# Kernel optimization log

Measured on AMD Instinct MI355X. Metric: run time of the kernel, lower is better.

The kernel has to match this reference:

```python
import jax, jax.numpy as jnp
import numpy as np

S = 4096      # total packed tokens
B = 8         # number of variable-length segments
E = 1152      # embed_dim (SigLIP2 so400m)
H = 16        # num_heads
D = E // H    # head_dim = 72


def setup_inputs() -> dict:
    key = jax.random.key(0)
    ks = jax.random.split(key, 8)
    w_std = 0.02
    theta = jax.random.uniform(ks[1], (S, D), jnp.float32, 0.0, 2.0 * np.pi)
    return {
        "hidden_states": jax.random.normal(ks[0], (S, E), jnp.float32),
        "cu_seqlens": jnp.arange(B + 1, dtype=jnp.int32) * (S // B),
        "cos": jnp.cos(theta),
        "sin": jnp.sin(theta),
        "Wq": jax.random.normal(ks[2], (E, E), jnp.float32) * w_std,
        "bq": jnp.zeros((E,), jnp.float32),
        "Wk": jax.random.normal(ks[3], (E, E), jnp.float32) * w_std,
        "bk": jnp.zeros((E,), jnp.float32),
        "Wv": jax.random.normal(ks[4], (E, E), jnp.float32) * w_std,
        "bv": jnp.zeros((E,), jnp.float32),
        "Wo": jax.random.normal(ks[5], (E, E), jnp.float32) * w_std,
        "bo": jnp.zeros((E,), jnp.float32),
    }


def _rotate_half(x):
    x1, x2 = jnp.split(x, 2, axis=-1)
    return jnp.concatenate((-x2, x1), axis=-1)


def reference(hidden_states, cu_seqlens, cos, sin, Wq, bq, Wk, bk, Wv, bv, Wo, bo):
    seq_len = hidden_states.shape[0]
    scale = np.float32(D) ** -0.5
    # projections -> [S, H, D]
    q = (hidden_states @ Wq.T + bq).reshape(seq_len, H, D)
    k = (hidden_states @ Wk.T + bk).reshape(seq_len, H, D)
    v = (hidden_states @ Wv.T + bv).reshape(seq_len, H, D)
    # inline RoPE (apply_rotary_pos_emb_vision): cos/sin broadcast over heads
    c = cos[:, None, :]
    s = sin[:, None, :]
    q = q * c + _rotate_half(q) * s
    k = k * c + _rotate_half(k) * s
    # segment id per token from cu_seqlens; block-diagonal attention mask
    seg = jnp.searchsorted(cu_seqlens[1:], jnp.arange(seq_len, dtype=cu_seqlens.dtype), side="right")
    mask = seg[:, None] == seg[None, :]                     # [S, S]
    scores = jnp.einsum("shd,thd->hst", q, k) * scale       # [H, S, S]
    neg = jnp.finfo(scores.dtype).min
    scores = jnp.where(mask[None, :, :], scores, neg)
    probs = jax.nn.softmax(scores, axis=-1)
    attn = jnp.einsum("hst,thd->shd", probs, v).reshape(seq_len, E)
    return attn @ Wo.T + bo
```

## Files before the change

### kernel.cpp

```cpp
#include <hip/hip_runtime.h>
#include <float.h>

#define S_LEN 4096
#define E_DIM 1152
#define NH    16
#define HD    72
#define HD2   36
#define NQKV  3456

typedef __attribute__((ext_vector_type(4))) float f32x4;
typedef __attribute__((ext_vector_type(8))) _Float16 f16x8;

__device__ __forceinline__ unsigned short f2h(float f) {
    union { _Float16 h; unsigned short u; } c;
    c.h = (_Float16)f;
    return c.u;
}

__device__ __forceinline__ void gload_lds16(const unsigned short* g, unsigned short* l) {
    __builtin_amdgcn_global_load_lds(
        (const __attribute__((address_space(1))) unsigned int*)g,
        (__attribute__((address_space(3))) unsigned int*)l, 16, 0, 0);
}

__global__ __launch_bounds__(256)
void pack_f16(const float* __restrict__ hs, const float* __restrict__ wq,
              const float* __restrict__ wk, const float* __restrict__ wv,
              const float* __restrict__ wo,
              unsigned short* __restrict__ hs_h, unsigned short* __restrict__ wqkv_h,
              unsigned short* __restrict__ wo_h)
{
    const float* src; unsigned short* dst; int n4;
    const int WSZ = E_DIM * E_DIM;
    switch (blockIdx.z) {
        case 0: src = hs; dst = hs_h;             n4 = S_LEN * E_DIM / 4; break;
        case 1: src = wq; dst = wqkv_h;           n4 = WSZ / 4; break;
        case 2: src = wk; dst = wqkv_h + WSZ;     n4 = WSZ / 4; break;
        case 3: src = wv; dst = wqkv_h + 2 * WSZ; n4 = WSZ / 4; break;
        default: src = wo; dst = wo_h;            n4 = WSZ / 4; break;
    }
    for (int i = blockIdx.x * 256 + threadIdx.x; i < n4; i += gridDim.x * 256) {
        f32x4 x = ((const f32x4*)src)[i];
        ushort4 hv;
        hv.x = f2h(x[0]); hv.y = f2h(x[1]); hv.z = f2h(x[2]); hv.w = f2h(x[3]);
        ((ushort4*)dst)[i] = hv;
    }
}

__global__ __launch_bounds__(256, 4)
void gemm_qkv_f16(const unsigned short* __restrict__ Ah, const unsigned short* __restrict__ Wh,
                  const float* __restrict__ bq, const float* __restrict__ bk,
                  const float* __restrict__ bv,
                  float* __restrict__ oq, float* __restrict__ ok, float* __restrict__ ov)
{
    __shared__ unsigned short sA[128 * 64];
    __shared__ unsigned short sB[128 * 64];
    const int tid  = threadIdx.x;
    const int w    = tid >> 6, lane = tid & 63;
    const int quad = lane >> 4, m = lane & 15;
    const int wr   = w & 1,  wc = w >> 1;

    const int bid = blockIdx.x;
    const int lin = (bid & 7) * 108 + (bid >> 3);
    const int n_t = lin >> 5;
    const int m_t = lin & 31;
    const int m0  = m_t * 128;
    const int n0  = n_t * 128;

    const int srow = lane >> 3;
    const int skc  = (lane & 7) ^ srow;

    f32x4 acc[4][4];
    #pragma unroll
    for (int i = 0; i < 4; ++i)
        #pragma unroll
        for (int j = 0; j < 4; ++j) acc[i][j] = (f32x4){0.f, 0.f, 0.f, 0.f};

    const int rm7 = m & 7;

    for (int k0 = 0; k0 < E_DIM; k0 += 64) {
        #pragma unroll
        for (int c = 0; c < 4; ++c) {
            int r = 32 * w + 8 * c + srow;
            gload_lds16(Ah + (size_t)(m0 + r) * E_DIM + k0 + skc * 8, &sA[(32 * w + 8 * c) * 64]);
            gload_lds16(Wh + (size_t)(n0 + r) * E_DIM + k0 + skc * 8, &sB[(32 * w + 8 * c) * 64]);
        }
        __syncthreads();

        #pragma unroll
        for (int k3 = 0; k3 < 2; ++k3) {
            f16x8 ah[4], bh[4];
            #pragma unroll
            for (int t = 0; t < 4; ++t) {
                int pc = ((k3 << 2) + quad) ^ rm7;
                ah[t] = *(const f16x8*)&sA[(64 * wr + 16 * t + m) * 64 + pc * 8];
                bh[t] = *(const f16x8*)&sB[(64 * wc + 16 * t + m) * 64 + pc * 8];
            }
            #pragma unroll
            for (int rt = 0; rt < 4; ++rt)
                #pragma unroll
                for (int ct = 0; ct < 4; ++ct)
                    acc[rt][ct] = __builtin_amdgcn_mfma_f32_16x16x32_f16(ah[rt], bh[ct], acc[rt][ct], 0, 0, 0);
        }
        __syncthreads();
    }

    const int which = n0 / E_DIM;
    const int n0l = n0 - which * E_DIM;
    const float* bp = (which == 0) ? bq : (which == 1) ? bk : bv;
    float* Cp       = (which == 0) ? oq : (which == 1) ? ok : ov;
    #pragma unroll
    for (int ct = 0; ct < 4; ++ct) {
        int col = n0l + 64 * wc + 16 * ct + m;
        float bias = bp[col];
        #pragma unroll
        for (int rt = 0; rt < 4; ++rt)
            #pragma unroll
            for (int reg = 0; reg < 4; ++reg) {
                int row = m0 + 64 * wr + 16 * rt + 4 * quad + reg;
                Cp[(size_t)row * E_DIM + col] = acc[rt][ct][reg] + bias;
            }
    }
}

__global__ __launch_bounds__(256, 4)
void gemm_out_f16(const unsigned short* __restrict__ Ah, const unsigned short* __restrict__ Wh,
                  const float* __restrict__ bo, float* __restrict__ Cp)
{
    __shared__ unsigned short sA[64 * 64];
    __shared__ unsigned short sB[128 * 64];
    const int tid  = threadIdx.x;
    const int w    = tid >> 6, lane = tid & 63;
    const int quad = lane >> 4, m = lane & 15;
    const int m0   = blockIdx.y * 64;
    const int n0   = blockIdx.x * 128;

    const int srow = lane >> 3;
    const int skc  = (lane & 7) ^ srow;

    f32x4 acc[4][2];
    #pragma unroll
    for (int i = 0; i < 4; ++i)
        #pragma unroll
        for (int j = 0; j < 2; ++j) acc[i][j] = (f32x4){0.f, 0.f, 0.f, 0.f};

    const int rm7 = m & 7;

    for (int k0 = 0; k0 < E_DIM; k0 += 64) {
        #pragma unroll
        for (int c = 0; c < 2; ++c) {
            int r = 16 * w + 8 * c + srow;
            gload_lds16(Ah + (size_t)(m0 + r) * E_DIM + k0 + skc * 8, &sA[(16 * w + 8 * c) * 64]);
        }
        #pragma unroll
        for (int c = 0; c < 4; ++c) {
            int r = 32 * w + 8 * c + srow;
            gload_lds16(Wh + (size_t)(n0 + r) * E_DIM + k0 + skc * 8, &sB[(32 * w + 8 * c) * 64]);
        }
        __syncthreads();
        #pragma unroll
        for (int k3 = 0; k3 < 2; ++k3) {
            f16x8 ah[4], bh[2];
            int pc = ((k3 << 2) + quad) ^ rm7;
            #pragma unroll
            for (int t = 0; t < 4; ++t)
                ah[t] = *(const f16x8*)&sA[(16 * t + m) * 64 + pc * 8];
            #pragma unroll
            for (int ct = 0; ct < 2; ++ct)
                bh[ct] = *(const f16x8*)&sB[(32 * w + 16 * ct + m) * 64 + pc * 8];
            #pragma unroll
            for (int rt = 0; rt < 4; ++rt)
                #pragma unroll
                for (int ct = 0; ct < 2; ++ct)
                    acc[rt][ct] = __builtin_amdgcn_mfma_f32_16x16x32_f16(ah[rt], bh[ct], acc[rt][ct], 0, 0, 0);
        }
        __syncthreads();
    }

    #pragma unroll
    for (int ct = 0; ct < 2; ++ct) {
        int col = n0 + 32 * w + 16 * ct + m;
        float bias = bo[col];
        #pragma unroll
        for (int rt = 0; rt < 4; ++rt)
            #pragma unroll
            for (int reg = 0; reg < 4; ++reg) {
                int row = m0 + 16 * rt + 4 * quad + reg;
                Cp[(size_t)row * E_DIM + col] = acc[rt][ct][reg] + bias;
            }
    }
}

__global__ __launch_bounds__(256)
void prep_kv(const float* __restrict__ kf, const float* __restrict__ vf,
             const float* __restrict__ cosb, const float* __restrict__ sinb,
             unsigned short* __restrict__ kh, unsigned short* __restrict__ vt)
{
    __shared__ unsigned short tile[HD][72];
    const int h  = blockIdx.y;
    const int s0 = blockIdx.x * 64;

    if (blockIdx.z == 0) {
        for (int task = threadIdx.x; task < 64 * 9; task += 256) {
            int row = task / 9, d0 = (task % 9) << 2;
            int s = s0 + row;
            const float* xr = kf + (size_t)s * E_DIM + h * HD;
            f32x4 a  = *(const f32x4*)(xr + d0);
            f32x4 b  = *(const f32x4*)(xr + d0 + HD2);
            f32x4 c1 = *(const f32x4*)(cosb + (size_t)s * HD + d0);
            f32x4 s1 = *(const f32x4*)(sinb + (size_t)s * HD + d0);
            f32x4 c2 = *(const f32x4*)(cosb + (size_t)s * HD + d0 + HD2);
            f32x4 s2 = *(const f32x4*)(sinb + (size_t)s * HD + d0 + HD2);
            f32x4 r1 = a * c1 - b * s1;
            f32x4 r2 = b * c2 + a * s2;
            uint2 u1, u2;
            u1.x = (unsigned)f2h(r1[0]) | ((unsigned)f2h(r1[1]) << 16);
            u1.y = (unsigned)f2h(r1[2]) | ((unsigned)f2h(r1[3]) << 16);
            u2.x = (unsigned)f2h(r2[0]) | ((unsigned)f2h(r2[1]) << 16);
            u2.y = (unsigned)f2h(r2[2]) | ((unsigned)f2h(r2[3]) << 16);
            unsigned short* orow = kh + ((size_t)h * S_LEN + s) * HD;
            *(uint2*)&orow[d0]       = u1;
            *(uint2*)&orow[d0 + HD2] = u2;
        }
    } else {
        for (int task = threadIdx.x; task < 64 * 18; task += 256) {
            int r = task / 18, c = task % 18;
            f32x4 x = *(const f32x4*)(vf + (size_t)(s0 + r) * E_DIM + h * HD + (c << 2));
            tile[(c << 2) + 0][r] = f2h(x[0]);
            tile[(c << 2) + 1][r] = f2h(x[1]);
            tile[(c << 2) + 2][r] = f2h(x[2]);
            tile[(c << 2) + 3][r] = f2h(x[3]);
        }
        __syncthreads();
        for (int task = threadIdx.x; task < HD * 8; task += 256) {
            int d = task / 8, cc = task % 8;
            uint4 val = *(const uint4*)&tile[d][cc << 3];
            *(uint4*)(vt + ((size_t)h * HD + d) * S_LEN + s0 + (cc << 3)) = val;
        }
    }
}

__global__ __launch_bounds__(256, 4)
void attn_f16(const float* __restrict__ qf, const float* __restrict__ cosb,
              const float* __restrict__ sinb, const unsigned short* __restrict__ kh,
              const unsigned short* __restrict__ vt, const int* __restrict__ cu,
              int nseg, unsigned short* __restrict__ out)
{
    __shared__ unsigned short ks_s[64][72];
    __shared__ unsigned short vs_s[80][72];
    __shared__ unsigned short ss_s[64][72];

    const int tid  = threadIdx.x;
    const int w    = tid >> 6;
    const int lane = tid & 63;
    const int quad = lane >> 4;
    const int m    = lane & 15;
    const int h    = blockIdx.y;
    const int qb0  = blockIdx.x * 64;
    const float cexp = 0.17002324f;

    {
        uint4 zz = make_uint4(0u, 0u, 0u, 0u);
        if (tid < 72) {
            int r = 72 + tid / 9, c = tid % 9;
            *(uint4*)&vs_s[r][c << 3] = zz;
        }
    }

    int rs_r[4], re_r[4];
    #pragma unroll
    for (int reg = 0; reg < 4; ++reg) {
        int row = qb0 + 16 * w + 4 * quad + reg;
        int st = 0;
        for (int i = 1; i < nseg; ++i) if (cu[i] <= row) st = i;
        rs_r[reg] = cu[st];
        re_r[reg] = cu[st + 1];
    }
    int st0 = 0, st1 = 0;
    for (int i = 1; i < nseg; ++i) {
        if (cu[i] <= qb0) st0 = i;
        if (cu[i] <= qb0 + 63) st1 = i;
    }
    const int kstart = cu[st0];
    const int kend   = cu[st1 + 1];
    const bool aligned = (st0 == st1);

    const unsigned short* ktbase = kh + (size_t)h * S_LEN * HD;
    const unsigned short* vtbase = vt + (size_t)h * HD * S_LEN;
    unsigned short* ksf = &ks_s[0][0];

    const int sl0 = tid, sl1 = tid + 256;
    const int sl2 = (tid < 64) ? tid + 512 : tid + 256;
    const int vd0 = sl0 >> 3, vc0 = (sl0 & 7) << 3;
    const int vd1 = sl1 >> 3, vc1 = (sl1 & 7) << 3;
    const int vd2 = sl2 >> 3, vc2 = (sl2 & 7) << 3;

    uint4 kp0, kp1, kp2, vp0, vp1, vp2;
    {
        const unsigned short* kt = ktbase + (size_t)kstart * HD;
        kp0 = *(const uint4*)(kt + sl0 * 8);
        kp1 = *(const uint4*)(kt + sl1 * 8);
        kp2 = *(const uint4*)(kt + sl2 * 8);
        vp0 = *(const uint4*)(vtbase + (size_t)vd0 * S_LEN + kstart + vc0);
        vp1 = *(const uint4*)(vtbase + (size_t)vd1 * S_LEN + kstart + vc1);
        vp2 = *(const uint4*)(vtbase + (size_t)vd2 * S_LEN + kstart + vc2);
    }

    for (int task = tid; task < 64 * 9; task += 256) {
        int row = task / 9, d0 = (task % 9) << 2;
        int s = qb0 + row;
        const float* xr = qf + (size_t)s * E_DIM + h * HD;
        f32x4 a  = *(const f32x4*)(xr + d0);
        f32x4 b  = *(const f32x4*)(xr + d0 + HD2);
        f32x4 c1 = *(const f32x4*)(cosb + (size_t)s * HD + d0);
        f32x4 s1 = *(const f32x4*)(sinb + (size_t)s * HD + d0);
        f32x4 c2 = *(const f32x4*)(cosb + (size_t)s * HD + d0 + HD2);
        f32x4 s2 = *(const f32x4*)(sinb + (size_t)s * HD + d0 + HD2);
        f32x4 r1 = a * c1 - b * s1;
        f32x4 r2 = b * c2 + a * s2;
        uint2 u1, u2;
        u1.x = (unsigned)f2h(r1[0]) | ((unsigned)f2h(r1[1]) << 16);
        u1.y = (unsigned)f2h(r1[2]) | ((unsigned)f2h(r1[3]) << 16);
        u2.x = (unsigned)f2h(r2[0]) | ((unsigned)f2h(r2[1]) << 16);
        u2.y = (unsigned)f2h(r2[2]) | ((unsigned)f2h(r2[3]) << 16);
        *(uint2*)&ks_s[row][d0]       = u1;
        *(uint2*)&ks_s[row][d0 + HD2] = u2;
    }
    __syncthreads();

    f16x8 qfr[3];
    {
        const unsigned short* qrow = &ks_s[16 * w + m][0];
        #pragma unroll
        for (int k3 = 0; k3 < 3; ++k3) {
            bool pad = (k3 == 2) && (quad != 0);
            int off = pad ? 0 : (k3 * 32 + quad * 8);
            f16x8 val = *(const f16x8*)(qrow + off);
            f16x8 z = {0, 0, 0, 0, 0, 0, 0, 0};
            qfr[k3] = pad ? z : val;
        }
    }

    f32x4 acc_o[5];
    #pragma unroll
    for (int i = 0; i < 5; ++i) acc_o[i] = (f32x4){0.f, 0.f, 0.f, 0.f};
    float l_r[4] = {0.f, 0.f, 0.f, 0.f};

    for (int kb = kstart; kb < kend; kb += 64) {
        __syncthreads();
        *(uint4*)(ksf + sl0 * 8) = kp0;
        *(uint4*)(ksf + sl1 * 8) = kp1;
        if (tid < 64) *(uint4*)(ksf + sl2 * 8) = kp2;
        *(uint4*)&vs_s[vd0][vc0] = vp0;
        *(uint4*)&vs_s[vd1][vc1] = vp1;
        if (tid < 64) *(uint4*)&vs_s[vd2][vc2] = vp2;
        __syncthreads();

        int kn = kb + 64;
        if (kn < kend) {
            const unsigned short* kt = ktbase + (size_t)kn * HD;
            kp0 = *(const uint4*)(kt + sl0 * 8);
            kp1 = *(const uint4*)(kt + sl1 * 8);
            kp2 = *(const uint4*)(kt + sl2 * 8);
            vp0 = *(const uint4*)(vtbase + (size_t)vd0 * S_LEN + kn + vc0);
            vp1 = *(const uint4*)(vtbase + (size_t)vd1 * S_LEN + kn + vc1);
            vp2 = *(const uint4*)(vtbase + (size_t)vd2 * S_LEN + kn + vc2);
        }

        f32x4 sacc[4];
        #pragma unroll
        for (int ct = 0; ct < 4; ++ct) sacc[ct] = (f32x4){0.f, 0.f, 0.f, 0.f};
        #pragma unroll
        for (int ct = 0; ct < 4; ++ct) {
            const unsigned short* krow = &ks_s[16 * ct + m][0];
            #pragma unroll
            for (int k3 = 0; k3 < 3; ++k3) {
                bool pad = (k3 == 2) && (quad != 0);
                int off = pad ? 0 : (k3 * 32 + quad * 8);
                f16x8 bfr = *(const f16x8*)(krow + off);
                f16x8 z = {0, 0, 0, 0, 0, 0, 0, 0};
                bfr = pad ? z : bfr;
                sacc[ct] = __builtin_amdgcn_mfma_f32_16x16x32_f16(qfr[k3], bfr, sacc[ct], 0, 0, 0);
            }
        }

        if (aligned) {
            #pragma unroll
            for (int ct = 0; ct < 4; ++ct)
                #pragma unroll
                for (int reg = 0; reg < 4; ++reg) {
                    float p = __builtin_amdgcn_exp2f(sacc[ct][reg] * cexp);
                    l_r[reg] += p;
                    ss_s[16 * w + 4 * quad + reg][16 * ct + m] = f2h(p);
                }
        } else {
            #pragma unroll
            for (int ct = 0; ct < 4; ++ct) {
                int key = kb + 16 * ct + m;
                #pragma unroll
                for (int reg = 0; reg < 4; ++reg) {
                    bool valid = (key >= rs_r[reg]) && (key < re_r[reg]);
                    float p = valid ? __builtin_amdgcn_exp2f(sacc[ct][reg] * cexp) : 0.f;
                    l_r[reg] += p;
                    ss_s[16 * w + 4 * quad + reg][16 * ct + m] = f2h(p);
                }
            }
        }

        {
            const unsigned short* prow = &ss_s[16 * w + m][0];
            f16x8 pf0 = *(const f16x8*)(prow + quad * 8);
            f16x8 pf1 = *(const f16x8*)(prow + 32 + quad * 8);
            #pragma unroll
            for (int ct2 = 0; ct2 < 5; ++ct2) {
                const unsigned short* vrow = &vs_s[16 * ct2 + m][0];
                f16x8 vf0 = *(const f16x8*)(vrow + quad * 8);
                f16x8 vf1 = *(const f16x8*)(vrow + 32 + quad * 8);
                acc_o[ct2] = __builtin_amdgcn_mfma_f32_16x16x32_f16(pf0, vf0, acc_o[ct2], 0, 0, 0);
                acc_o[ct2] = __builtin_amdgcn_mfma_f32_16x16x32_f16(pf1, vf1, acc_o[ct2], 0, 0, 0);
            }
        }
    }

    #pragma unroll
    for (int reg = 0; reg < 4; ++reg) {
        float l = l_r[reg];
        l += __shfl_xor(l, 1);
        l += __shfl_xor(l, 2);
        l += __shfl_xor(l, 4);
        l += __shfl_xor(l, 8);
        l_r[reg] = l;
    }

    #pragma unroll
    for (int reg = 0; reg < 4; ++reg) {
        float linv = (l_r[reg] > 0.f) ? 1.f / l_r[reg] : 0.f;
        int row = qb0 + 16 * w + 4 * quad + reg;
        unsigned short* orow = out + (size_t)row * E_DIM + h * HD;
        #pragma unroll
        for (int ct2 = 0; ct2 < 5; ++ct2) {
            int col = 16 * ct2 + m;
            if (col < HD) orow[col] = f2h(acc_o[ct2][reg] * linv);
        }
    }
}

extern "C" void kernel_launch(void* const* d_in, const int* in_sizes, int n_in,
                              void* d_out, int out_size, void* d_ws, size_t ws_size,
                              hipStream_t stream)
{
    const float* hs   = (const float*)d_in[0];
    const int*   cu   = (const int*)d_in[1];
    const float* cosb = (const float*)d_in[2];
    const float* sinb = (const float*)d_in[3];
    const float* Wq   = (const float*)d_in[4];
    const float* bq   = (const float*)d_in[5];
    const float* Wk   = (const float*)d_in[6];
    const float* bk   = (const float*)d_in[7];
    const float* Wv   = (const float*)d_in[8];
    const float* bv   = (const float*)d_in[9];
    const float* Wo   = (const float*)d_in[10];
    const float* bo   = (const float*)d_in[11];
    float* outp = (float*)d_out;

    const size_t mat = (size_t)S_LEN * E_DIM;
    float* qf = (float*)d_ws;
    float* kf = qf + mat;
    float* vf = kf + mat;
    unsigned short* hs_h   = (unsigned short*)(vf + mat);
    unsigned short* wqkv_h = hs_h + mat;
    unsigned short* wo_h   = wqkv_h + (size_t)NQKV * E_DIM;
    unsigned short* vtb    = wo_h + (size_t)E_DIM * E_DIM;
    unsigned short* kh     = hs_h;
    unsigned short* attn_h = (unsigned short*)vf;

    const int nseg = in_sizes[1] - 1;

    dim3 gpack(512, 1, 5);
    pack_f16<<<gpack, 256, 0, stream>>>(hs, Wq, Wk, Wv, Wo, hs_h, wqkv_h, wo_h);

    gemm_qkv_f16<<<dim3(864), 256, 0, stream>>>(hs_h, wqkv_h, bq, bk, bv, qf, kf, vf);

    dim3 gprep(S_LEN / 64, NH, 2);
    prep_kv<<<gprep, 256, 0, stream>>>(kf, vf, cosb, sinb, kh, vtb);

    dim3 gattn(S_LEN / 64, NH, 1);
    attn_f16<<<gattn, 256, 0, stream>>>(qf, cosb, sinb, kh, vtb, cu, nseg, attn_h);

    dim3 gout(E_DIM / 128, S_LEN / 64, 1);
    gemm_out_f16<<<gout, 256, 0, stream>>>(attn_h, wo_h, bo, outp);
}
```

Measured before the change: 208.7 us.

## Rewrite QKV GEMM with 256x256 double-buffered tiles and a fused QKV output layout

The QKV projection GEMM now uses 512-thread blocks computing 256x256 tiles, with double-buffered LDS so the next K-slice's global-to-LDS loads overlap the current MFMA work. It uses explicit vmcnt waits, barriers and s_setprio around the MFMA bursts. Q, K and V are written into a single interleaved [S, 3456] fp32 buffer. The attention output is placed in the already-consumed V columns with a matching stride, and downstream kernels are re-indexed accordingly. The larger LDS footprint (about 128KB) limits each CU to one block, and the last N tile is partly wasted on padding rows.

```diff
diff --git a/kernel.cpp b/kernel.cpp
--- a/kernel.cpp
+++ b/kernel.cpp
@@ -7,6 +7,8 @@
 #define HD    72
 #define HD2   36
 #define NQKV  3456
+#define QKVP  3456
+#define AH_STRIDE 6912
 
 typedef __attribute__((ext_vector_type(4))) float f32x4;
 typedef __attribute__((ext_vector_type(8))) _Float16 f16x8;
@@ -47,79 +49,107 @@
     }
 }
 
-__global__ __launch_bounds__(256, 4)
-void gemm_qkv_f16(const unsigned short* __restrict__ Ah, const unsigned short* __restrict__ Wh,
+__global__ __launch_bounds__(512, 2)
+void gemm_qkv_8ph(const unsigned short* __restrict__ Ah, const unsigned short* __restrict__ Wh,
                   const float* __restrict__ bq, const float* __restrict__ bk,
-                  const float* __restrict__ bv,
-                  float* __restrict__ oq, float* __restrict__ ok, float* __restrict__ ov)
+                  const float* __restrict__ bv, float* __restrict__ C)
 {
-    __shared__ unsigned short sA[128 * 64];
-    __shared__ unsigned short sB[128 * 64];
+    __shared__ unsigned short sA[2][256 * 64];
+    __shared__ unsigned short sB[2][256 * 64];
+
     const int tid  = threadIdx.x;
     const int w    = tid >> 6, lane = tid & 63;
     const int quad = lane >> 4, m = lane & 15;
-    const int wr   = w & 1,  wc = w >> 1;
+    const int wm   = w >> 2,  wn = w & 3;
 
     const int bid = blockIdx.x;
-    const int lin = (bid & 7) * 108 + (bid >> 3);
-    const int n_t = lin >> 5;
-    const int m_t = lin & 31;
-    const int m0  = m_t * 128;
-    const int n0  = n_t * 128;
+    const int lin = (bid & 7) * 28 + (bid >> 3);
+    const int n_t = lin >> 4;
+    const int m_t = lin & 15;
+    const int m0  = m_t * 256;
+    const int n0  = n_t * 256;
 
     const int srow = lane >> 3;
     const int skc  = (lane & 7) ^ srow;
-
-    f32x4 acc[4][4];
-    #pragma unroll
-    for (int i = 0; i < 4; ++i)
+    const int rm7  = m & 7;
+
+    f32x4 acc[8][4];
+    #pragma unroll
+    for (int i = 0; i < 8; ++i)
         #pragma unroll
         for (int j = 0; j < 4; ++j) acc[i][j] = (f32x4){0.f, 0.f, 0.f, 0.f};
 
-    const int rm7 = m & 7;
-
-    for (int k0 = 0; k0 < E_DIM; k0 += 64) {
-        #pragma unroll
-        for (int c = 0; c < 4; ++c) {
-            int r = 32 * w + 8 * c + srow;
-            gload_lds16(Ah + (size_t)(m0 + r) * E_DIM + k0 + skc * 8, &sA[(32 * w + 8 * c) * 64]);
-            gload_lds16(Wh + (size_t)(n0 + r) * E_DIM + k0 + skc * 8, &sB[(32 * w + 8 * c) * 64]);
-        }
-        __syncthreads();
-
-        #pragma unroll
-        for (int k3 = 0; k3 < 2; ++k3) {
-            f16x8 ah[4], bh[4];
-            #pragma unroll
-            for (int t = 0; t < 4; ++t) {
-                int pc = ((k3 << 2) + quad) ^ rm7;
-                ah[t] = *(const f16x8*)&sA[(64 * wr + 16 * t + m) * 64 + pc * 8];
-                bh[t] = *(const f16x8*)&sB[(64 * wc + 16 * t + m) * 64 + pc * 8];
-            }
-            #pragma unroll
-            for (int rt = 0; rt < 4; ++rt)
+#define STAGE(buf, k0)                                                                 \
+    {                                                                                  \
+        _Pragma("unroll")                                                              \
+        for (int s = 0; s < 4; ++s) {                                                  \
+            int rr = s * 64 + w * 8 + srow;                                            \
+            gload_lds16(Ah + (size_t)(m0 + rr) * E_DIM + (k0) + skc * 8,               \
+                        &sA[buf][(s * 64 + w * 8) * 64]);                              \
+            gload_lds16(Wh + (size_t)(n0 + rr) * E_DIM + (k0) + skc * 8,               \
+                        &sB[buf][(s * 64 + w * 8) * 64]);                              \
+        }                                                                              \
+    }
+
+#define COMPUTE(buf)                                                                   \
+    {                                                                                  \
+        _Pragma("unroll")                                                              \
+        for (int k3 = 0; k3 < 2; ++k3) {                                               \
+            f16x8 ah[8], bh[4];                                                        \
+            int pc = ((k3 << 2) + quad) ^ rm7;                                         \
+            _Pragma("unroll")                                                          \
+            for (int rt = 0; rt < 8; ++rt)                                             \
+                ah[rt] = *(const f16x8*)&sA[buf][(wm * 128 + 16 * rt + m) * 64 + pc * 8]; \
+            _Pragma("unroll")                                                          \
+            for (int ct = 0; ct < 4; ++ct)                                             \
+                bh[ct] = *(const f16x8*)&sB[buf][(wn * 64 + 16 * ct + m) * 64 + pc * 8];  \
+            __builtin_amdgcn_s_setprio(1);                                             \
+            _Pragma("unroll")                                                          \
+            for (int rt = 0; rt < 8; ++rt)                                             \
+                _Pragma("unroll")                                                      \
+                for (int ct = 0; ct < 4; ++ct)                                         \
+                    acc[rt][ct] = __builtin_amdgcn_mfma_f32_16x16x32_f16(ah[rt], bh[ct], acc[rt][ct], 0, 0, 0); \
+            __builtin_amdgcn_s_setprio(0);                                             \
+        }                                                                              \
+    }
+
+    const int NT = E_DIM / 64;
+    STAGE(0, 0);
+    for (int i = 0; i < NT - 1; ++i) {
+        STAGE((i + 1) & 1, (i + 1) * 64);
+        asm volatile("s_waitcnt vmcnt(8)" ::: "memory");
+        __builtin_amdgcn_sched_barrier(0);
+        __builtin_amdgcn_s_barrier();
+        __builtin_amdgcn_sched_barrier(0);
+        COMPUTE(i & 1);
+        __builtin_amdgcn_sched_barrier(0);
+        __builtin_amdgcn_s_barrier();
+        __builtin_amdgcn_sched_barrier(0);
+    }
+    asm volatile("s_waitcnt vmcnt(0)" ::: "memory");
+    __builtin_amdgcn_sched_barrier(0);
+    __builtin_amdgcn_s_barrier();
+    __builtin_amdgcn_sched_barrier(0);
+    COMPUTE((NT - 1) & 1);
+#undef STAGE
+#undef COMPUTE
+
+    #pragma unroll
+    for (int ct = 0; ct < 4; ++ct) {
+        int colb = n0 + wn * 64 + 16 * ct;
+        if (colb < NQKV) {
+            int col = colb + m;
+            int which = col / E_DIM;
+            const float* bp = (which == 0) ? bq : (which == 1) ? bk : bv;
+            float bias = bp[col - which * E_DIM];
+            #pragma unroll
+            for (int rt = 0; rt < 8; ++rt)
                 #pragma unroll
-                for (int ct = 0; ct < 4; ++ct)
-                    acc[rt][ct] = __builtin_amdgcn_mfma_f32_16x16x32_f16(ah[rt], bh[ct], acc[rt][ct], 0, 0, 0);
-        }
-        __syncthreads();
-    }
-
-    const int which = n0 / E_DIM;
-    const int n0l = n0 - which * E_DIM;
-    const float* bp = (which == 0) ? bq : (which == 1) ? bk : bv;
-    float* Cp       = (which == 0) ? oq : (which == 1) ? ok : ov;
-    #pragma unroll
-    for (int ct = 0; ct < 4; ++ct) {
-        int col = n0l + 64 * wc + 16 * ct + m;
-        float bias = bp[col];
-        #pragma unroll
-        for (int rt = 0; rt < 4; ++rt)
-            #pragma unroll
-            for (int reg = 0; reg < 4; ++reg) {
-                int row = m0 + 64 * wr + 16 * rt + 4 * quad + reg;
-                Cp[(size_t)row * E_DIM + col] = acc[rt][ct][reg] + bias;
-            }
+                for (int reg = 0; reg < 4; ++reg) {
+                    int row = m0 + wm * 128 + 16 * rt + 4 * quad + reg;
+                    C[(size_t)row * QKVP + col] = acc[rt][ct][reg] + bias;
+                }
+        }
     }
 }
 
@@ -150,7 +180,7 @@
         #pragma unroll
         for (int c = 0; c < 2; ++c) {
             int r = 16 * w + 8 * c + srow;
-            gload_lds16(Ah + (size_t)(m0 + r) * E_DIM + k0 + skc * 8, &sA[(16 * w + 8 * c) * 64]);
+            gload_lds16(Ah + (size_t)(m0 + r) * AH_STRIDE + k0 + skc * 8, &sA[(16 * w + 8 * c) * 64]);
         }
         #pragma unroll
         for (int c = 0; c < 4; ++c) {
@@ -204,7 +234,7 @@
         for (int task = threadIdx.x; task < 64 * 9; task += 256) {
             int row = task / 9, d0 = (task % 9) << 2;
             int s = s0 + row;
-            const float* xr = kf + (size_t)s * E_DIM + h * HD;
+            const float* xr = kf + (size_t)s * QKVP + h * HD;
             f32x4 a  = *(const f32x4*)(xr + d0);
             f32x4 b  = *(const f32x4*)(xr + d0 + HD2);
             f32x4 c1 = *(const f32x4*)(cosb + (size_t)s * HD + d0);
@@ -225,7 +255,7 @@
     } else {
         for (int task = threadIdx.x; task < 64 * 18; task += 256) {
             int r = task / 18, c = task % 18;
-            f32x4 x = *(const f32x4*)(vf + (size_t)(s0 + r) * E_DIM + h * HD + (c << 2));
+            f32x4 x = *(const f32x4*)(vf + (size_t)(s0 + r) * QKVP + h * HD + (c << 2));
             tile[(c << 2) + 0][r] = f2h(x[0]);
             tile[(c << 2) + 1][r] = f2h(x[1]);
             tile[(c << 2) + 2][r] = f2h(x[2]);
@@ -309,7 +339,7 @@
     for (int task = tid; task < 64 * 9; task += 256) {
         int row = task / 9, d0 = (task % 9) << 2;
         int s = qb0 + row;
-        const float* xr = qf + (size_t)s * E_DIM + h * HD;
+        const float* xr = qf + (size_t)s * QKVP + h * HD;
         f32x4 a  = *(const f32x4*)(xr + d0);
         f32x4 b  = *(const f32x4*)(xr + d0 + HD2);
         f32x4 c1 = *(const f32x4*)(cosb + (size_t)s * HD + d0);
@@ -436,7 +466,7 @@
     for (int reg = 0; reg < 4; ++reg) {
         float linv = (l_r[reg] > 0.f) ? 1.f / l_r[reg] : 0.f;
         int row = qb0 + 16 * w + 4 * quad + reg;
-        unsigned short* orow = out + (size_t)row * E_DIM + h * HD;
+        unsigned short* orow = out + (size_t)row * AH_STRIDE + h * HD;
         #pragma unroll
         for (int ct2 = 0; ct2 < 5; ++ct2) {
             int col = 16 * ct2 + m;
@@ -464,22 +494,24 @@
     float* outp = (float*)d_out;
 
     const size_t mat = (size_t)S_LEN * E_DIM;
-    float* qf = (float*)d_ws;
-    float* kf = qf + mat;
-    float* vf = kf + mat;
-    unsigned short* hs_h   = (unsigned short*)(vf + mat);
+    float* o_qkv = (float*)d_ws;
+    unsigned short* hs_h   = (unsigned short*)(o_qkv + (size_t)S_LEN * QKVP);
     unsigned short* wqkv_h = hs_h + mat;
-    unsigned short* wo_h   = wqkv_h + (size_t)NQKV * E_DIM;
+    unsigned short* wo_h   = wqkv_h + (size_t)3584 * E_DIM;
     unsigned short* vtb    = wo_h + (size_t)E_DIM * E_DIM;
     unsigned short* kh     = hs_h;
-    unsigned short* attn_h = (unsigned short*)vf;
+    unsigned short* attn_h = (unsigned short*)o_qkv + 4608;
+
+    const float* qf = o_qkv;
+    const float* kf = o_qkv + E_DIM;
+    const float* vf = o_qkv + 2 * E_DIM;
 
     const int nseg = in_sizes[1] - 1;
 
     dim3 gpack(512, 1, 5);
     pack_f16<<<gpack, 256, 0, stream>>>(hs, Wq, Wk, Wv, Wo, hs_h, wqkv_h, wo_h);
 
-    gemm_qkv_f16<<<dim3(864), 256, 0, stream>>>(hs_h, wqkv_h, bq, bk, bv, qf, kf, vf);
+    gemm_qkv_8ph<<<dim3(224), 512, 0, stream>>>(hs_h, wqkv_h, bq, bk, bv, o_qkv);
 
     dim3 gprep(S_LEN / 64, NH, 2);
     prep_kv<<<gprep, 256, 0, stream>>>(kf, vf, cosb, sinb, kh, vtb);
```

Result: slower. 215.1 us (+3.1%).
